# Kernel tuning notes

Measured on AMD Instinct MI355X. Metric: run time of the kernel, lower is better.

The kernel has to match this reference:

```python
import jax, jax.numpy as jnp
import numpy as np

B, N, C, CO = 256, 80, 1024, 1024
SLOPE = 0.2
BN_EPS = 1e-5

def leaky(x):
    return jax.nn.leaky_relu(x, SLOPE)

def setup_inputs() -> dict:
    key = jax.random.key(0)
    ks = jax.random.split(key, 8)
    stdv = 1.0 / np.sqrt(C)
    return {
        "x": jax.random.normal(ks[0], (B, N, C), jnp.float32),
        "out1": jax.random.normal(ks[1], (B, N), jnp.float32),
        "A": jax.random.uniform(ks[2], (N, N), jnp.float32, 0.05, 1.0),
        "static_weight": jax.random.uniform(ks[3], (C, C), jnp.float32, -stdv, stdv),
        "conv_g_w": jax.random.normal(ks[4], (C, C), jnp.float32) * 0.02,
        "conv_g_b": jnp.zeros((C,), jnp.float32),
        "bn_gamma": jnp.ones((C,), jnp.float32),
        "bn_beta": jnp.zeros((C,), jnp.float32),
        "conv_co_w": jax.random.normal(ks[5], (N, 2 * C), jnp.float32) * 0.02,
        "conv_co_b": jnp.zeros((N,), jnp.float32),
        "dynamic_weight": jax.random.uniform(ks[6], (C, CO), jnp.float32, -stdv, stdv),
    }

def _gen_adj(A):
    # D = diag(rowsum(A)^-0.5); adj = (A @ D).T @ D = D A^T D
    d = jnp.power(A.sum(1), -0.5)
    return d[:, None] * A.T * d[None, :]

def _gen_adjs(A):
    # batched version of _gen_adj; A: [B,N,N]
    d = jnp.power(A.sum(2), -0.5)  # [B,N]
    return d[:, :, None] * jnp.swapaxes(A, 1, 2) * d[:, None, :]

def reference(x, out1, A, static_weight, conv_g_w, conv_g_b, bn_gamma, bn_beta, conv_co_w, conv_co_b, dynamic_weight):
    n = x.shape[1]
    # static GCN + residual
    adj_s = _gen_adj(A)
    h = leaky(jnp.einsum('ij,bjc->bic', adj_s, x))
    x = x + h @ static_weight
    # construct dynamic graph
    xt = jnp.swapaxes(x, 1, 2)                      # [B,C,N]
    glb = xt.mean(2)                                # adaptive avg pool -> [B,C]
    glb = glb @ conv_g_w.T + conv_g_b               # 1x1 conv
    mu = glb.mean(0)
    var = glb.var(0)                                # biased, training-mode BN
    glb = (glb - mu) * jax.lax.rsqrt(var + BN_EPS) * bn_gamma + bn_beta
    glb = leaky(glb)
    cat = jnp.concatenate([jnp.broadcast_to(glb[:, :, None], xt.shape), xt], axis=1)  # [B,2C,N]
    dyn = jax.nn.sigmoid(jnp.einsum('nk,bkm->bnm', conv_co_w, cat) + conv_co_b[None, :, None])  # [B,N,N]
    # adjacency consistency loss
    out1s = jax.nn.sigmoid(out1)
    t = jnp.einsum('bn,bnm->bm', out1s, dyn) / n
    loss = jnp.sum(jnp.linalg.norm(out1s - t, axis=1))
    # dynamic GCN
    adjs = _gen_adjs(dyn)
    h = leaky(jnp.einsum('bnm,bmc->bnc', adjs, x))
    out = leaky(h @ dynamic_weight)
    return out, loss
```

## Files before the change

### kernel.cpp

```cpp
#include <hip/hip_runtime.h>
#include <hip/hip_bf16.h>
#include <math.h>

#define B_  256
#define N_  80
#define C_  1024
#define CO_ 1024

typedef __hip_bfloat16 bf16;
using bf16x8 = __attribute__((ext_vector_type(8))) short;
using f32x4  = __attribute__((ext_vector_type(4))) float;

__device__ __forceinline__ float leaky(float v){ return v >= 0.f ? v : 0.2f * v; }
__device__ __forceinline__ float sigmoidf_(float v){ return 1.f / (1.f + __expf(-v)); }

__device__ __forceinline__ void gll16(const void* g, void* l){
    __builtin_amdgcn_global_load_lds(
        (const __attribute__((address_space(1))) void*)g,
        (__attribute__((address_space(3))) void*)l, 16, 0, 0);
}

__global__ __launch_bounds__(256) void k_convT2(const float* __restrict__ W0, const float* __restrict__ W1,
                                                bf16* __restrict__ T0, bf16* __restrict__ T1){
    __shared__ float t[32][33];
    const float* W = blockIdx.z ? W1 : W0;
    bf16* WT = blockIdx.z ? T1 : T0;
    int k0 = blockIdx.y * 32, n0 = blockIdx.x * 32;
    int tx = threadIdx.x & 31, ty = threadIdx.x >> 5;
    for (int i = ty; i < 32; i += 8) t[i][tx] = W[(size_t)(k0 + i) * 1024 + n0 + tx];
    __syncthreads();
    for (int i = ty; i < 32; i += 8)
        WT[(size_t)(n0 + i) * 1024 + k0 + tx] = __float2bfloat16(t[tx][i]);
}

__global__ void k_cvt_ccw(const float* __restrict__ ccw, bf16* __restrict__ ccwb){
    int i = blockIdx.x * 256 + threadIdx.x;
    ccwb[i] = __float2bfloat16(ccw[i]);
}
__global__ void k_cvt4(const float* __restrict__ src, bf16* __restrict__ dst){
    int i = (blockIdx.x * 256 + threadIdx.x) * 4;
    float4 v = *(const float4*)(src + i);
    dst[i + 0] = __float2bfloat16(v.x);
    dst[i + 1] = __float2bfloat16(v.y);
    dst[i + 2] = __float2bfloat16(v.z);
    dst[i + 3] = __float2bfloat16(v.w);
}

__global__ void k_adj(const float* __restrict__ A, bf16* __restrict__ adjb){
    __shared__ float d[N_];
    int t = threadIdx.x;
    if (t < N_){
        float s = 0.f;
        for (int j = 0; j < N_; j++) s += A[t * N_ + j];
        d[t] = rsqrtf(s);
    }
    __syncthreads();
    for (int idx = t; idx < N_ * N_; idx += 256){
        int i = idx / N_, j = idx - i * N_;
        adjb[i * 88 + j] = __float2bfloat16(d[i] * A[j * N_ + i] * d[j]);
    }
}

template<int MODE>
__global__ __launch_bounds__(256) void k_prop_mfma(const void* __restrict__ srcv,
                                                   const bf16* __restrict__ Ag_,
                                                   bf16* __restrict__ H){
    __shared__ bf16 Btl[256 * 88];
    __shared__ bf16 Al [80 * 88];
    int b = blockIdx.x, c0 = blockIdx.y * 256, tid = threadIdx.x;
    int wave = tid >> 6, lane = tid & 63;
    int l15 = lane & 15, hi = lane >> 4;

    const bf16* Ag = Ag_ + (MODE ? (size_t)b * 80 * 88 : 0);
    #pragma unroll
    for (int k = 0; k < 4; k++){
        int cb = wave * 64 + 256 * k;
        if (cb + lane < 880)
            gll16(Ag + (size_t)(cb + lane) * 8, Al + (size_t)cb * 8);
    }
    {
        size_t rowbase = (size_t)b * 81920 + c0 + tid;
        #pragma unroll 8
        for (int m = 0; m < 80; m++){
            bf16 h;
            if (MODE == 0) h = __float2bfloat16(((const float*)srcv)[rowbase + (size_t)m * 1024]);
            else           h = ((const bf16*)srcv)[rowbase + (size_t)m * 1024];
            Btl[tid * 88 + m] = h;
        }
    }
    __syncthreads();

    f32x4 acc[5][4];
    #pragma unroll
    for (int i = 0; i < 5; i++)
        #pragma unroll
        for (int j = 0; j < 4; j++) acc[i][j] = (f32x4){0.f, 0.f, 0.f, 0.f};

    #pragma unroll
    for (int ks = 0; ks < 3; ks++){
        bf16x8 a[5], bv[4];
        if (ks < 2){
            int k0 = ks * 32;
            #pragma unroll
            for (int i = 0; i < 5; i++)
                a[i] = *(const bf16x8*)(Al + (i * 16 + l15) * 88 + k0 + hi * 8);
            #pragma unroll
            for (int j = 0; j < 4; j++)
                bv[j] = *(const bf16x8*)(Btl + (wave * 64 + j * 16 + l15) * 88 + k0 + hi * 8);
        } else {
            int koff = (hi < 2) ? 64 + hi * 8 : 0;
            #pragma unroll
            for (int i = 0; i < 5; i++){
                bf16x8 v = *(const bf16x8*)(Al + (i * 16 + l15) * 88 + koff);
                if (hi >= 2) v = 0;
                a[i] = v;
            }
            #pragma unroll
            for (int j = 0; j < 4; j++){
                bf16x8 v = *(const bf16x8*)(Btl + (wave * 64 + j * 16 + l15) * 88 + koff);
                if (hi >= 2) v = 0;
                bv[j] = v;
            }
        }
        #pragma unroll
        for (int i = 0; i < 5; i++)
            #pragma unroll
            for (int j = 0; j < 4; j++)
                acc[i][j] = __builtin_amdgcn_mfma_f32_16x16x32_bf16(a[i], bv[j], acc[i][j], 0, 0, 0);
    }

    #pragma unroll
    for (int i = 0; i < 5; i++){
        #pragma unroll
        for (int r = 0; r < 4; r++){
            int orow = i * 16 + hi * 4 + r;
            #pragma unroll
            for (int j = 0; j < 4; j++){
                int ocol = c0 + wave * 64 + j * 16 + l15;
                H[(size_t)b * 81920 + (size_t)orow * 1024 + ocol] =
                    __float2bfloat16(leaky(acc[i][j][r]));
            }
        }
    }
}

template<int EPI>
__global__ __launch_bounds__(256) void k_gemm_mfma(const bf16* __restrict__ Abf,
                                                   const bf16* __restrict__ WT,
                                                   const float* __restrict__ Res,
                                                   void* __restrict__ Outv){
    __shared__ alignas(16) bf16 As[3][128 * 32];
    __shared__ alignas(16) bf16 Bs[3][128 * 32];
    const int K = 1024;
    const int NT = 32;
    int tid = threadIdx.x;
    int wave = tid >> 6, lane = tid & 63;
    int l15 = lane & 15, hi = lane >> 4;

    int bid = blockIdx.x;
    int xcd = bid & 7, idx = bid >> 3;
    int row0 = (xcd * 20 + (idx >> 3)) * 128;
    int col0 = (idx & 7) * 128;

    int sr = tid >> 2;
    int sq = (tid & 3) ^ ((tid >> 3) & 3);
    const bf16* gA = Abf + (size_t)(row0 + sr) * K + sq * 8;
    const bf16* gB = WT  + (size_t)(col0 + sr) * K + sq * 8;

    int wr = (wave >> 1) * 64, wc = (wave & 1) * 64;
    int soff = (hi ^ ((l15 >> 1) & 3)) * 8;

    f32x4 acc[4][4];
    #pragma unroll
    for (int i = 0; i < 4; i++)
        #pragma unroll
        for (int j = 0; j < 4; j++) acc[i][j] = (f32x4){0.f, 0.f, 0.f, 0.f};

    auto STAGE = [&](int t){
        int buf = t % 3;
        int k0 = t * 32;
        bf16* da = &As[buf][wave * 512];
        bf16* db = &Bs[buf][wave * 512];
        gll16(gA + k0, da);
        gll16(gA + (size_t)64 * K + k0, da + 2048);
        gll16(gB + k0, db);
        gll16(gB + (size_t)64 * K + k0, db + 2048);
    };

    STAGE(0);
    STAGE(1);
    for (int t = 0; t < NT; ++t){
        if (t == NT - 1) asm volatile("s_waitcnt vmcnt(0)" ::: "memory");
        else             asm volatile("s_waitcnt vmcnt(4)" ::: "memory");
        __builtin_amdgcn_s_barrier();
        if (t + 2 < NT) STAGE(t + 2);
        int buf = t % 3;
        const bf16* pa = &As[buf][0] + (wr + l15) * 32 + soff;
        const bf16* pb = &Bs[buf][0] + (wc + l15) * 32 + soff;
        bf16x8 a[4], b[4];
        #pragma unroll
        for (int i = 0; i < 4; i++) a[i] = *(const bf16x8*)(pa + i * 512);
        #pragma unroll
        for (int j = 0; j < 4; j++) b[j] = *(const bf16x8*)(pb + j * 512);
        __builtin_amdgcn_s_setprio(1);
        #pragma unroll
        for (int i = 0; i < 4; i++)
            #pragma unroll
            for (int j = 0; j < 4; j++)
                acc[i][j] = __builtin_amdgcn_mfma_f32_16x16x32_bf16(a[i], b[j], acc[i][j], 0, 0, 0);
        __builtin_amdgcn_s_setprio(0);
    }

    int orow = row0 + wr + hi * 4;
    int ocol = col0 + wc + l15;
    #pragma unroll
    for (int i = 0; i < 4; i++){
        #pragma unroll
        for (int r = 0; r < 4; r++){
            int rr = orow + i * 16 + r;
            #pragma unroll
            for (int j = 0; j < 4; j++){
                size_t o = (size_t)rr * 1024 + ocol + j * 16;
                float v = acc[i][j][r];
                if (EPI == 0) ((bf16*)Outv)[o] = __float2bfloat16(v + Res[o]);
                else          ((float*)Outv)[o] = leaky(v);
            }
        }
    }
}

__global__ __launch_bounds__(256) void k_gemm_glb(const bf16* __restrict__ Abf,
                                                  const bf16* __restrict__ Bw,
                                                  const float* __restrict__ bias,
                                                  float* __restrict__ Out){
    __shared__ alignas(16) bf16 As[3][128 * 32];
    __shared__ alignas(16) bf16 Bs[3][128 * 32];
    const int K = 1024;
    const int NT = 32;
    int tid = threadIdx.x;
    int wave = tid >> 6, lane = tid & 63;
    int l15 = lane & 15, hi = lane >> 4;

    int row0 = (blockIdx.x >> 3) * 128;
    int col0 = (blockIdx.x & 7) * 128;

    int sr = tid >> 2;
    int sq = (tid & 3) ^ ((tid >> 3) & 3);
    const bf16* gA = Abf + (size_t)(row0 + sr) * K + sq * 8;
    const bf16* gB = Bw  + (size_t)(col0 + sr) * K + sq * 8;

    int wr = (wave >> 1) * 64, wc = (wave & 1) * 64;
    int soff = (hi ^ ((l15 >> 1) & 3)) * 8;

    f32x4 acc[4][4];
    #pragma unroll
    for (int i = 0; i < 4; i++)
        #pragma unroll
        for (int j = 0; j < 4; j++) acc[i][j] = (f32x4){0.f, 0.f, 0.f, 0.f};

    auto STAGE = [&](int t){
        int buf = t % 3;
        int k0 = t * 32;
        bf16* da = &As[buf][wave * 512];
        bf16* db = &Bs[buf][wave * 512];
        gll16(gA + k0, da);
        gll16(gA + (size_t)64 * K + k0, da + 2048);
        gll16(gB + k0, db);
        gll16(gB + (size_t)64 * K + k0, db + 2048);
    };

    STAGE(0);
    STAGE(1);
    for (int t = 0; t < NT; ++t){
        if (t == NT - 1) asm volatile("s_waitcnt vmcnt(0)" ::: "memory");
        else             asm volatile("s_waitcnt vmcnt(4)" ::: "memory");
        __builtin_amdgcn_s_barrier();
        if (t + 2 < NT) STAGE(t + 2);
        int buf = t % 3;
        const bf16* pa = &As[buf][0] + (wr + l15) * 32 + soff;
        const bf16* pb = &Bs[buf][0] + (wc + l15) * 32 + soff;
        bf16x8 a[4], b[4];
        #pragma unroll
        for (int i = 0; i < 4; i++) a[i] = *(const bf16x8*)(pa + i * 512);
        #pragma unroll
        for (int j = 0; j < 4; j++) b[j] = *(const bf16x8*)(pb + j * 512);
        #pragma unroll
        for (int i = 0; i < 4; i++)
            #pragma unroll
            for (int j = 0; j < 4; j++)
                acc[i][j] = __builtin_amdgcn_mfma_f32_16x16x32_bf16(a[i], b[j], acc[i][j], 0, 0, 0);
    }

    int orow = row0 + wr + hi * 4;
    int ocol = col0 + wc + l15;
    #pragma unroll
    for (int i = 0; i < 4; i++){
        #pragma unroll
        for (int r = 0; r < 4; r++){
            int rr = orow + i * 16 + r;
            #pragma unroll
            for (int j = 0; j < 4; j++){
                int cl = ocol + j * 16;
                Out[(size_t)rr * 1024 + cl] = acc[i][j][r] + bias[cl];
            }
        }
    }
}

__global__ void k_pool(const bf16* __restrict__ X2b, bf16* __restrict__ glb0b){
    int b = blockIdx.x, c = blockIdx.y * 256 + threadIdx.x;
    const bf16* p = X2b + (size_t)b * 81920 + c;
    float s = 0.f;
    for (int nn = 0; nn < N_; nn++) s += __bfloat162float(p[nn * 1024]);
    glb0b[b * C_ + c] = __float2bfloat16(s * (1.f / N_));
}

__global__ __launch_bounds__(256) void k_bnstat(const float* __restrict__ g, float* __restrict__ mu,
                                                float* __restrict__ rstd){
    __shared__ float rs[8][32], rs2[8][32];
    int tid = threadIdx.x;
    int c = blockIdx.x * 32 + (tid & 31);
    int grp = tid >> 5;
    float s = 0.f, s2 = 0.f;
    for (int bb = 0; bb < 32; bb++){
        float v = g[(size_t)(grp * 32 + bb) * 1024 + c];
        s += v; s2 += v * v;
    }
    rs[grp][tid & 31] = s;
    rs2[grp][tid & 31] = s2;
    __syncthreads();
    if (tid < 32){
        float S = 0.f, S2 = 0.f;
        #pragma unroll
        for (int q = 0; q < 8; q++){ S += rs[q][tid]; S2 += rs2[q][tid]; }
        float m = S * (1.f / B_);
        float var = S2 * (1.f / B_) - m * m;
        int cc = blockIdx.x * 32 + tid;
        mu[cc] = m;
        rstd[cc] = rsqrtf(var + 1e-5f);
    }
}

__global__ void k_bnapply(const float* __restrict__ g, const float* __restrict__ mu,
                          const float* __restrict__ rstd, const float* __restrict__ gamma,
                          const float* __restrict__ beta, bf16* __restrict__ o){
    int i = blockIdx.x * 256 + threadIdx.x;
    int c = i & (C_ - 1);
    float v = (g[i] - mu[c]) * rstd[c] * gamma[c] + beta[c];
    o[i] = __float2bfloat16(leaky(v));
}

__global__ __launch_bounds__(320) void k_dyn_fused(const bf16* __restrict__ X2b,
                                                   const bf16* __restrict__ ccwb,
                                                   const bf16* __restrict__ glb2b,
                                                   const float* __restrict__ ccb,
                                                   const float* __restrict__ out1,
                                                   bf16* __restrict__ ADJD,
                                                   float* __restrict__ lossp){
    __shared__ float S[80][81];
    __shared__ float di_s[80], o1s[80], dd[80];
    int b = blockIdx.x, tid = threadIdx.x;
    int wave = tid >> 6, lane = tid & 63;
    int l15 = lane & 15, hi = lane >> 4;

    const bf16* arow = ccwb + (size_t)(wave * 16 + l15) * 2048 + hi * 8;
    const bf16* gG = glb2b + (size_t)b * 1024 + hi * 8;
    const bf16* gX = X2b + (size_t)b * 81920 + hi * 8;

    f32x4 acc[5];
    #pragma unroll
    for (int j = 0; j < 5; j++) acc[j] = (f32x4){0.f, 0.f, 0.f, 0.f};

    #pragma unroll 8
    for (int k0 = 0; k0 < 1024; k0 += 32){
        bf16x8 a = *(const bf16x8*)(arow + k0);
        bf16x8 g = *(const bf16x8*)(gG + k0);
        #pragma unroll
        for (int j = 0; j < 5; j++)
            acc[j] = __builtin_amdgcn_mfma_f32_16x16x32_bf16(a, g, acc[j], 0, 0, 0);
    }
    #pragma unroll 4
    for (int k0 = 0; k0 < 1024; k0 += 32){
        bf16x8 a = *(const bf16x8*)(arow + 1024 + k0);
        #pragma unroll
        for (int j = 0; j < 5; j++){
            bf16x8 bv = *(const bf16x8*)(gX + (size_t)(j * 16 + l15) * 1024 + k0);
            acc[j] = __builtin_amdgcn_mfma_f32_16x16x32_bf16(a, bv, acc[j], 0, 0, 0);
        }
    }

    #pragma unroll
    for (int r = 0; r < 4; r++){
        int n = wave * 16 + hi * 4 + r;
        float cb = ccb[n];
        #pragma unroll
        for (int j = 0; j < 5; j++)
            S[n][j * 16 + l15] = sigmoidf_(acc[j][r] + cb);
    }
    __syncthreads();
    if (tid < 80){
        float rsum = 0.f;
        for (int m = 0; m < 80; m++) rsum += S[tid][m];
        di_s[tid] = rsqrtf(rsum);
        o1s[tid] = sigmoidf_(out1[b * 80 + tid]);
    }
    __syncthreads();
    if (tid < 80){
        float cs = 0.f;
        for (int n = 0; n < 80; n++) cs += o1s[n] * S[n][tid];
        float diff = o1s[tid] - cs * (1.f / 80.f);
        dd[tid] = diff * diff;
    }
    __syncthreads();
    if (tid == 0){
        float s = 0.f;
        for (int m = 0; m < 80; m++) s += dd[m];
        lossp[b] = sqrtf(s);
    }
    bf16* ab = ADJD + (size_t)b * 80 * 88;
    for (int idx = tid; idx < 6400; idx += 320){
        int n = idx / 80, m = idx - n * 80;
        ab[n * 88 + m] = __float2bfloat16(di_s[n] * S[m][n] * di_s[m]);
    }
}

__global__ void k_lsum(const float* __restrict__ lossp, float* __restrict__ out_loss){
    float v = lossp[threadIdx.x];
    for (int off = 32; off; off >>= 1) v += __shfl_down(v, off);
    __shared__ float wsum[4];
    int lane = threadIdx.x & 63, w = threadIdx.x >> 6;
    if (lane == 0) wsum[w] = v;
    __syncthreads();
    if (threadIdx.x == 0) out_loss[0] = wsum[0] + wsum[1] + wsum[2] + wsum[3];
}

extern "C" void kernel_launch(void* const* d_in, const int* in_sizes, int n_in,
                              void* d_out, int out_size, void* d_ws, size_t ws_size,
                              hipStream_t stream) {
    const float* x     = (const float*)d_in[0];
    const float* out1  = (const float*)d_in[1];
    const float* A     = (const float*)d_in[2];
    const float* sw    = (const float*)d_in[3];
    const float* cgw   = (const float*)d_in[4];
    const float* cgb   = (const float*)d_in[5];
    const float* gamma = (const float*)d_in[6];
    const float* beta  = (const float*)d_in[7];
    const float* ccw   = (const float*)d_in[8];
    const float* ccb   = (const float*)d_in[9];
    const float* dw    = (const float*)d_in[10];
    float* out = (float*)d_out;

    const size_t XN = (size_t)B_ * N_ * C_;
    char* p = (char*)d_ws;
    bf16*  Hbf  = (bf16*)p;   p += XN * 2;
    bf16*  X2b  = (bf16*)p;   p += XN * 2;
    bf16*  SWT  = (bf16*)p;   p += (size_t)C_ * C_ * 2;
    bf16*  DWT  = (bf16*)p;   p += (size_t)C_ * CO_ * 2;
    bf16*  CCWB = (bf16*)p;   p += (size_t)N_ * 2048 * 2;
    bf16*  CGWB = (bf16*)p;   p += (size_t)C_ * C_ * 2;
    bf16*  ADJS = (bf16*)p;   p += (size_t)80 * 88 * 2;
    bf16*  ADJD = (bf16*)p;   p += (size_t)B_ * 80 * 88 * 2;
    bf16*  GLB0 = (bf16*)p;   p += (size_t)B_ * C_ * 2;
    float* GLB1 = (float*)p;  p += (size_t)B_ * C_ * 4;
    bf16*  GLB2 = (bf16*)p;   p += (size_t)B_ * C_ * 2;
    float* MU   = (float*)p;  p += C_ * 4;
    float* RSTD = (float*)p;  p += C_ * 4;
    float* LOSSP= (float*)p;  p += B_ * 4;

    k_convT2<<<dim3(32, 32, 2), 256, 0, stream>>>(sw, dw, SWT, DWT);
    k_cvt_ccw<<<(N_ * 2048) / 256, 256, 0, stream>>>(ccw, CCWB);
    k_cvt4<<<(C_ * C_) / 1024, 256, 0, stream>>>(cgw, CGWB);
    k_adj<<<1, 256, 0, stream>>>(A, ADJS);
    k_prop_mfma<0><<<dim3(B_, 4), 256, 0, stream>>>(x, ADJS, Hbf);
    k_gemm_mfma<0><<<1280, 256, 0, stream>>>(Hbf, SWT, x, X2b);
    k_pool<<<dim3(B_, C_ / 256), 256, 0, stream>>>(X2b, GLB0);
    k_gemm_glb<<<16, 256, 0, stream>>>(GLB0, CGWB, cgb, GLB1);
    k_bnstat<<<32, 256, 0, stream>>>(GLB1, MU, RSTD);
    k_bnapply<<<(B_ * C_) / 256, 256, 0, stream>>>(GLB1, MU, RSTD, gamma, beta, GLB2);
    k_dyn_fused<<<B_, 320, 0, stream>>>(X2b, CCWB, GLB2, ccb, out1, ADJD, LOSSP);
    k_lsum<<<1, 256, 0, stream>>>(LOSSP, out + (size_t)B_ * N_ * CO_);
    k_prop_mfma<1><<<dim3(B_, 4), 256, 0, stream>>>(X2b, ADJD, Hbf);
    k_gemm_mfma<1><<<1280, 256, 0, stream>>>(Hbf, DWT, nullptr, out);
}
```

Measured before the change: 272.5 us.

## Load GEMM A operand straight to registers and vectorize pooling reads

The main 1280-block GEMM no longer stages the A tile through LDS. Each wave loads its A fragments directly from global memory into registers, double-buffered across k-steps, and only B goes through a 4-deep LDS ring with adjusted vmcnt waits. This halves LDS traffic and LDS footprint per block, which may raise occupancy, but A reads become per-lane 16-byte strided global loads whose latency must be hidden by the register prefetch. The pooling kernel now reads 8 bf16 channels per thread with vector loads instead of scalar loads.

Measured after the change: 325.1 us. 19.3% more time.

```diff
diff --git a/kernel.cpp b/kernel.cpp
--- a/kernel.cpp
+++ b/kernel.cpp
@@ -149,6 +149,96 @@
                                                    const bf16* __restrict__ WT,
                                                    const float* __restrict__ Res,
                                                    void* __restrict__ Outv){
+    __shared__ alignas(16) bf16 Bs[4][128 * 32];
+    const int K = 1024;
+    const int NT = 32;
+    int tid = threadIdx.x;
+    int wave = tid >> 6, lane = tid & 63;
+    int l15 = lane & 15, hi = lane >> 4;
+
+    int bid = blockIdx.x;
+    int xcd = bid & 7, idx = bid >> 3;
+    int row0 = (xcd * 20 + (idx >> 3)) * 128;
+    int col0 = (idx & 7) * 128;
+
+    int sr = tid >> 2;
+    int sq = (tid & 3) ^ ((tid >> 3) & 3);
+    const bf16* gB = WT + (size_t)(col0 + sr) * K + sq * 8;
+
+    int wr = (wave >> 1) * 64, wc = (wave & 1) * 64;
+    int soff = (hi ^ ((l15 >> 1) & 3)) * 8;
+
+    const bf16* gA = Abf + (size_t)(row0 + wr + l15) * K + hi * 8;
+
+    f32x4 acc[4][4];
+    #pragma unroll
+    for (int i = 0; i < 4; i++)
+        #pragma unroll
+        for (int j = 0; j < 4; j++) acc[i][j] = (f32x4){0.f, 0.f, 0.f, 0.f};
+
+    auto STAGE_B = [&](int t){
+        bf16* db = &Bs[t & 3][wave * 512];
+        gll16(gB + t * 32, db);
+        gll16(gB + (size_t)64 * K + t * 32, db + 2048);
+    };
+
+    bf16x8 a0[4], a1[4];
+    STAGE_B(0); STAGE_B(1); STAGE_B(2);
+    #pragma unroll
+    for (int i = 0; i < 4; i++)
+        a0[i] = *(const bf16x8*)(gA + (size_t)i * 16 * K);
+
+    auto kstep = [&](int t, bf16x8 (&cur)[4], bf16x8 (&nxt)[4]){
+        __builtin_amdgcn_s_barrier();
+        if (t + 3 < NT) STAGE_B(t + 3);
+        if (t + 1 < NT){
+            #pragma unroll
+            for (int i = 0; i < 4; i++)
+                nxt[i] = *(const bf16x8*)(gA + (size_t)i * 16 * K + (t + 1) * 32);
+        }
+        if (t < NT - 3)      asm volatile("s_waitcnt vmcnt(6)" ::: "memory");
+        else if (t < NT - 1) asm volatile("s_waitcnt vmcnt(4)" ::: "memory");
+        else                 asm volatile("s_waitcnt vmcnt(0)" ::: "memory");
+        const bf16* pb = &Bs[t & 3][0] + (wc + l15) * 32 + soff;
+        bf16x8 b[4];
+        #pragma unroll
+        for (int j = 0; j < 4; j++) b[j] = *(const bf16x8*)(pb + j * 512);
+        __builtin_amdgcn_s_setprio(1);
+        #pragma unroll
+        for (int i = 0; i < 4; i++)
+            #pragma unroll
+            for (int j = 0; j < 4; j++)
+                acc[i][j] = __builtin_amdgcn_mfma_f32_16x16x32_bf16(cur[i], b[j], acc[i][j], 0, 0, 0);
+        __builtin_amdgcn_s_setprio(0);
+    };
+
+    for (int t0 = 0; t0 < NT; t0 += 2){
+        kstep(t0,     a0, a1);
+        kstep(t0 + 1, a1, a0);
+    }
+
+    int orow = row0 + wr + hi * 4;
+    int ocol = col0 + wc + l15;
+    #pragma unroll
+    for (int i = 0; i < 4; i++){
+        #pragma unroll
+        for (int r = 0; r < 4; r++){
+            int rr = orow + i * 16 + r;
+            #pragma unroll
+            for (int j = 0; j < 4; j++){
+                size_t o = (size_t)rr * 1024 + ocol + j * 16;
+                float v = acc[i][j][r];
+                if (EPI == 0) ((bf16*)Outv)[o] = __float2bfloat16(v + Res[o]);
+                else          ((float*)Outv)[o] = leaky(v);
+            }
+        }
+    }
+}
+
+__global__ __launch_bounds__(256) void k_gemm_glb(const bf16* __restrict__ Abf,
+                                                  const bf16* __restrict__ Bw,
+                                                  const float* __restrict__ bias,
+                                                  float* __restrict__ Out){
     __shared__ alignas(16) bf16 As[3][128 * 32];
     __shared__ alignas(16) bf16 Bs[3][128 * 32];
     const int K = 1024;
@@ -157,15 +247,13 @@
     int wave = tid >> 6, lane = tid & 63;
     int l15 = lane & 15, hi = lane >> 4;
 
-    int bid = blockIdx.x;
-    int xcd = bid & 7, idx = bid >> 3;
-    int row0 = (xcd * 20 + (idx >> 3)) * 128;
-    int col0 = (idx & 7) * 128;
+    int row0 = (blockIdx.x >> 3) * 128;
+    int col0 = (blockIdx.x & 7) * 128;
 
     int sr = tid >> 2;
     int sq = (tid & 3) ^ ((tid >> 3) & 3);
     const bf16* gA = Abf + (size_t)(row0 + sr) * K + sq * 8;
-    const bf16* gB = WT  + (size_t)(col0 + sr) * K + sq * 8;
+    const bf16* gB = Bw  + (size_t)(col0 + sr) * K + sq * 8;
 
     int wr = (wave >> 1) * 64, wc = (wave & 1) * 64;
     int soff = (hi ^ ((l15 >> 1) & 3)) * 8;
@@ -202,88 +290,6 @@
         for (int i = 0; i < 4; i++) a[i] = *(const bf16x8*)(pa + i * 512);
         #pragma unroll
         for (int j = 0; j < 4; j++) b[j] = *(const bf16x8*)(pb + j * 512);
-        __builtin_amdgcn_s_setprio(1);
-        #pragma unroll
-        for (int i = 0; i < 4; i++)
-            #pragma unroll
-            for (int j = 0; j < 4; j++)
-                acc[i][j] = __builtin_amdgcn_mfma_f32_16x16x32_bf16(a[i], b[j], acc[i][j], 0, 0, 0);
-        __builtin_amdgcn_s_setprio(0);
-    }
-
-    int orow = row0 + wr + hi * 4;
-    int ocol = col0 + wc + l15;
-    #pragma unroll
-    for (int i = 0; i < 4; i++){
-        #pragma unroll
-        for (int r = 0; r < 4; r++){
-            int rr = orow + i * 16 + r;
-            #pragma unroll
-            for (int j = 0; j < 4; j++){
-                size_t o = (size_t)rr * 1024 + ocol + j * 16;
-                float v = acc[i][j][r];
-                if (EPI == 0) ((bf16*)Outv)[o] = __float2bfloat16(v + Res[o]);
-                else          ((float*)Outv)[o] = leaky(v);
-            }
-        }
-    }
-}
-
-__global__ __launch_bounds__(256) void k_gemm_glb(const bf16* __restrict__ Abf,
-                                                  const bf16* __restrict__ Bw,
-                                                  const float* __restrict__ bias,
-                                                  float* __restrict__ Out){
-    __shared__ alignas(16) bf16 As[3][128 * 32];
-    __shared__ alignas(16) bf16 Bs[3][128 * 32];
-    const int K = 1024;
-    const int NT = 32;
-    int tid = threadIdx.x;
-    int wave = tid >> 6, lane = tid & 63;
-    int l15 = lane & 15, hi = lane >> 4;
-
-    int row0 = (blockIdx.x >> 3) * 128;
-    int col0 = (blockIdx.x & 7) * 128;
-
-    int sr = tid >> 2;
-    int sq = (tid & 3) ^ ((tid >> 3) & 3);
-    const bf16* gA = Abf + (size_t)(row0 + sr) * K + sq * 8;
-    const bf16* gB = Bw  + (size_t)(col0 + sr) * K + sq * 8;
-
-    int wr = (wave >> 1) * 64, wc = (wave & 1) * 64;
-    int soff = (hi ^ ((l15 >> 1) & 3)) * 8;
-
-    f32x4 acc[4][4];
-    #pragma unroll
-    for (int i = 0; i < 4; i++)
-        #pragma unroll
-        for (int j = 0; j < 4; j++) acc[i][j] = (f32x4){0.f, 0.f, 0.f, 0.f};
-
-    auto STAGE = [&](int t){
-        int buf = t % 3;
-        int k0 = t * 32;
-        bf16* da = &As[buf][wave * 512];
-        bf16* db = &Bs[buf][wave * 512];
-        gll16(gA + k0, da);
-        gll16(gA + (size_t)64 * K + k0, da + 2048);
-        gll16(gB + k0, db);
-        gll16(gB + (size_t)64 * K + k0, db + 2048);
-    };
-
-    STAGE(0);
-    STAGE(1);
-    for (int t = 0; t < NT; ++t){
-        if (t == NT - 1) asm volatile("s_waitcnt vmcnt(0)" ::: "memory");
-        else             asm volatile("s_waitcnt vmcnt(4)" ::: "memory");
-        __builtin_amdgcn_s_barrier();
-        if (t + 2 < NT) STAGE(t + 2);
-        int buf = t % 3;
-        const bf16* pa = &As[buf][0] + (wr + l15) * 32 + soff;
-        const bf16* pb = &Bs[buf][0] + (wc + l15) * 32 + soff;
-        bf16x8 a[4], b[4];
-        #pragma unroll
-        for (int i = 0; i < 4; i++) a[i] = *(const bf16x8*)(pa + i * 512);
-        #pragma unroll
-        for (int j = 0; j < 4; j++) b[j] = *(const bf16x8*)(pb + j * 512);
         #pragma unroll
         for (int i = 0; i < 4; i++)
             #pragma unroll
@@ -307,12 +313,19 @@
     }
 }
 
-__global__ void k_pool(const bf16* __restrict__ X2b, bf16* __restrict__ glb0b){
-    int b = blockIdx.x, c = blockIdx.y * 256 + threadIdx.x;
-    const bf16* p = X2b + (size_t)b * 81920 + c;
-    float s = 0.f;
-    for (int nn = 0; nn < N_; nn++) s += __bfloat162float(p[nn * 1024]);
-    glb0b[b * C_ + c] = __float2bfloat16(s * (1.f / N_));
+__global__ __launch_bounds__(128) void k_pool(const bf16* __restrict__ X2b, bf16* __restrict__ glb0b){
+    int b = blockIdx.x, c8 = threadIdx.x * 8;
+    const bf16* p = X2b + (size_t)b * 81920 + c8;
+    float s[8] = {0.f,0.f,0.f,0.f,0.f,0.f,0.f,0.f};
+    for (int nn = 0; nn < N_; nn++){
+        union { bf16x8 v; bf16 e[8]; } u;
+        u.v = *(const bf16x8*)(p + (size_t)nn * 1024);
+        #pragma unroll
+        for (int k = 0; k < 8; k++) s[k] += __bfloat162float(u.e[k]);
+    }
+    #pragma unroll
+    for (int k = 0; k < 8; k++)
+        glb0b[b * C_ + c8 + k] = __float2bfloat16(s[k] * (1.f / N_));
 }
 
 __global__ __launch_bounds__(256) void k_bnstat(const float* __restrict__ g, float* __restrict__ mu,
@@ -473,7 +486,7 @@
     k_adj<<<1, 256, 0, stream>>>(A, ADJS);
     k_prop_mfma<0><<<dim3(B_, 4), 256, 0, stream>>>(x, ADJS, Hbf);
     k_gemm_mfma<0><<<1280, 256, 0, stream>>>(Hbf, SWT, x, X2b);
-    k_pool<<<dim3(B_, C_ / 256), 256, 0, stream>>>(X2b, GLB0);
+    k_pool<<<B_, 128, 0, stream>>>(X2b, GLB0);
     k_gemm_glb<<<16, 256, 0, stream>>>(GLB0, CGWB, cgb, GLB1);
     k_bnstat<<<32, 256, 0, stream>>>(GLB1, MU, RSTD);
     k_bnapply<<<(B_ * C_) / 256, 256, 0, stream>>>(GLB1, MU, RSTD, gamma, beta, GLB2);
```
